# Optimization experiments

Measured on AMD Instinct MI355X. Metric: run time of the kernel, lower is better.

The kernel has to match this reference:

```python
import jax, jax.numpy as jnp
import numpy as np

HIDDEN = 512
HEADS = 8
HEAD_DIM = HIDDEN // HEADS
NUM_NODES = 512
NUM_EDGES = 16384
NEG_INF = -1e9


def setup_inputs() -> dict:
    key = jax.random.key(0)
    ks = jax.random.split(key, 8)
    x = jax.random.normal(ks[0], (4, 12, NUM_NODES, HIDDEN), dtype=jnp.float32)
    edge_index = jax.random.randint(ks[1], (2, NUM_EDGES), 0, NUM_NODES, dtype=jnp.int64)
    s = 1.0 / np.sqrt(HIDDEN)
    Wq = jax.random.uniform(ks[2], (HIDDEN, HIDDEN), jnp.float32, -s, s)
    Wk = jax.random.uniform(ks[3], (HIDDEN, HIDDEN), jnp.float32, -s, s)
    Wv = jax.random.uniform(ks[4], (HIDDEN, HIDDEN), jnp.float32, -s, s)
    bq = jax.random.uniform(ks[5], (HIDDEN,), jnp.float32, -s, s)
    bk = jax.random.uniform(ks[6], (HIDDEN,), jnp.float32, -s, s)
    bv = jax.random.uniform(ks[7], (HIDDEN,), jnp.float32, -s, s)
    return {"x": x, "edge_index": edge_index, "Wq": Wq, "bq": bq,
            "Wk": Wk, "bk": bk, "Wv": Wv, "bv": bv}


def reference(x, edge_index, Wq, bq, Wk, bk, Wv, bv):
    B, S, N, F = x.shape  # [batch, seq_len, num_nodes, features]
    xf = x.reshape(B * S, N, F)
    # torch nn.Linear: y = x @ W.T + b
    Q = xf @ Wq.T + bq
    K = xf @ Wk.T + bk
    V = xf @ Wv.T + bv
    # [B*S, heads, N, head_dim]
    Q = Q.reshape(B * S, N, HEADS, HEAD_DIM).transpose(0, 2, 1, 3)
    K = K.reshape(B * S, N, HEADS, HEAD_DIM).transpose(0, 2, 1, 3)
    V = V.reshape(B * S, N, HEADS, HEAD_DIM).transpose(0, 2, 1, 3)
    scores = jnp.einsum('bhnd,bhmd->bhnm', Q, K) / np.sqrt(HEAD_DIM)
    # static graph mask: 1 where edge exists
    mask = jnp.zeros((N, N), dtype=jnp.float32).at[edge_index[0], edge_index[1]].set(1.0)
    scores = jnp.where(mask[None, None] == 0, NEG_INF, scores)
    attn = jax.nn.softmax(scores, axis=-1)  # dropout is identity in eval
    out = jnp.einsum('bhnm,bhmd->bhnd', attn, V)
    out = out.transpose(0, 2, 1, 3).reshape(B, S, N, F)
    return out
```

## Files before the change

### kernel.cpp

```cpp
#include <hip/hip_runtime.h>
#include <hip/hip_bf16.h>

typedef __attribute__((ext_vector_type(8))) short short8;
typedef __attribute__((ext_vector_type(4))) float f32x4;
typedef __attribute__((ext_vector_type(4))) unsigned int u32x4;
typedef unsigned long long u64;
typedef unsigned short u16;
typedef unsigned int u32;

#define NODES 512
#define HIDDEN 512
#define NEDGES 16384

#define KOFF ((size_t)384 * 32 * 2 * 512)
#define VOFF ((size_t)2 * 384 * 32 * 2 * 512)

static __device__ __forceinline__ u16 f2bf(float f) {
  unsigned u = __float_as_uint(f);
  u += 0x7FFFu + ((u >> 16) & 1u);
  return (u16)(u >> 16);
}

static __device__ __forceinline__ void gld_lds16(const void* g, void* l) {
  __builtin_amdgcn_global_load_lds(
      (const __attribute__((address_space(1))) unsigned int*)g,
      (__attribute__((address_space(3))) unsigned int*)l, 16, 0, 0);
}

__global__ void cast_all(const float* __restrict__ x, const float* __restrict__ wq,
                         const float* __restrict__ wk, const float* __restrict__ wv,
                         u16* __restrict__ xb, u16* __restrict__ wb) {
  const int n4 = 3145728 + 196608;
  int stride = gridDim.x * blockDim.x;
  for (int i = blockIdx.x * blockDim.x + threadIdx.x; i < n4; i += stride) {
    float4 v;
    u16* dst;
    int di;
    if (i < 3145728) {
      v = reinterpret_cast<const float4*>(x)[i];
      dst = xb; di = i;
    } else {
      int t = i - 3145728;
      const float* src = (t < 65536) ? wq : (t < 131072) ? wk : wv;
      v = reinterpret_cast<const float4*>(src)[t & 65535];
      dst = wb; di = t;
    }
    ushort4 o;
    o.x = f2bf(v.x); o.y = f2bf(v.y); o.z = f2bf(v.z); o.w = f2bf(v.w);
    reinterpret_cast<ushort4*>(dst)[di] = o;
  }
}

__global__ void mask_scatter(const int* __restrict__ e, u64* __restrict__ bits) {
  int i = blockIdx.x * blockDim.x + threadIdx.x;
  if (i < NEDGES) {
    int src = e[i];
    int dst = e[NEDGES + i];
    atomicOr(&bits[src * 8 + (dst >> 6)], 1ull << (dst & 63));
  }
}

__global__ void mask_frag(const u64* __restrict__ bits, u32* __restrict__ mf) {
  int idx = blockIdx.x * 256 + threadIdx.x;
  int w = idx & 3;
  int lane = (idx >> 2) & 63;
  int hh = (idx >> 8) & 1;
  int kt = (idx >> 9) & 7;
  int qsg = idx >> 12;
  int q = qsg * 16 + (lane & 15);
  int bit = hh * 32 + (lane >> 4) * 8 + 2 * w;
  u64 row = bits[q * 8 + kt];
  u32 b0 = (u32)(row >> bit) & 1u;
  u32 b1 = (u32)(row >> (bit + 1)) & 1u;
  mf[idx] = (b0 ? 0xFFFFu : 0u) | (b1 ? 0xFFFF0000u : 0u);
}

__global__ __launch_bounds__(256, 2)
void qkv_gemm(const u16* __restrict__ xb, const u16* __restrict__ wb,
              const float* __restrict__ bq, const float* __restrict__ bk,
              const float* __restrict__ bv, u16* __restrict__ qkv) {
  __shared__ u16 As[2][128 * 64];
  __shared__ u16 Bs[2][128 * 64];

  const int blk = blockIdx.x;
  const int xcd = blk & 7;
  const int i = blk >> 3;
  const int m0 = ((i % 24) + xcd * 24) * 128;
  const int nz = i / 24;
  const int n0 = (nz & 3) * 128;
  const int z = nz >> 2;

  const u16* Wz = wb + (size_t)z * (512 * 512);
  const float* bias = (z == 0) ? bq : (z == 1) ? bk : bv;

  const int tid = threadIdx.x;
  const int lane = tid & 63;
  const int w = tid >> 6;
  const int wr = w >> 1, wc = w & 1;
  const int l = lane & 15, j = lane >> 4;
  const int sl = l & 7;
  const int kb = ((lane & 7) ^ (lane >> 3)) * 16;

#define STAGE(bb, kt_) do {                                                     \
    const int k0_ = (kt_) * 64;                                                 \
    _Pragma("unroll")                                                           \
    for (int t_ = 0; t_ < 4; ++t_) {                                            \
      int c_ = w * 4 + t_;                                                      \
      int row_ = c_ * 8 + (lane >> 3);                                          \
      gld_lds16((const char*)xb + ((size_t)(m0 + row_) * 512 + k0_) * 2 + kb,   \
                (char*)&As[bb][0] + c_ * 1024);                                 \
      gld_lds16((const char*)Wz + ((size_t)(n0 + row_) * 512 + k0_) * 2 + kb,   \
                (char*)&Bs[bb][0] + c_ * 1024);                                 \
    }                                                                           \
  } while (0)

  f32x4 acc[4][4] = {};

  STAGE(0, 0);
  int cur = 0;

  for (int kt = 0; kt < 8; ++kt) {
    if (kt < 7) {
      STAGE(cur ^ 1, kt + 1);
      asm volatile("s_waitcnt vmcnt(8)" ::: "memory");
    } else {
      asm volatile("s_waitcnt vmcnt(0)" ::: "memory");
    }
    __builtin_amdgcn_s_barrier();

#pragma unroll
    for (int kk = 0; kk < 2; ++kk) {
      short8 a[4], b[4];
#pragma unroll
      for (int mi = 0; mi < 4; ++mi)
        a[mi] = *(const short8*)(&As[cur][0] + (wr * 64 + mi * 16 + l) * 64 +
                                 (((kk * 4 + j) ^ sl) * 8));
#pragma unroll
      for (int ni = 0; ni < 4; ++ni)
        b[ni] = *(const short8*)(&Bs[cur][0] + (wc * 64 + ni * 16 + l) * 64 +
                                 (((kk * 4 + j) ^ sl) * 8));
      if (z == 2) {
#pragma unroll
        for (int mi = 0; mi < 4; ++mi)
#pragma unroll
          for (int ni = 0; ni < 4; ++ni)
            acc[mi][ni] = __builtin_amdgcn_mfma_f32_16x16x32_bf16(a[mi], b[ni], acc[mi][ni], 0, 0, 0);
      } else {
#pragma unroll
        for (int mi = 0; mi < 4; ++mi)
#pragma unroll
          for (int ni = 0; ni < 4; ++ni)
            acc[mi][ni] = __builtin_amdgcn_mfma_f32_16x16x32_bf16(b[ni], a[mi], acc[mi][ni], 0, 0, 0);
      }
    }

    if (kt < 7) {
      asm volatile("s_waitcnt lgkmcnt(0)" ::: "memory");
      __builtin_amdgcn_s_barrier();
    }
    cur ^= 1;
  }
#undef STAGE

  const int bs = m0 >> 9;
  const int hh = (n0 >> 6) + wc;
  const int bh = bs * 8 + hh;

  if (z == 2) {
    const int ktb = ((m0 & 511) >> 6) + wr;
#pragma unroll
    for (int ni = 0; ni < 4; ++ni) {
      int jcol = n0 + wc * 64 + ni * 16 + l;
      float bv_ = bias[jcol];
      int ds = ni;
#pragma unroll
      for (int mi = 0; mi < 4; ++mi) {
        int kk2 = mi >> 1, oct = ((mi & 1) << 1) | (j >> 1);
        ushort4 pk;
#pragma unroll
        for (int r = 0; r < 4; ++r) pk[r] = f2bf(acc[mi][ni][r] + bv_);
        size_t idx = VOFF + (((((size_t)bh * 8 + ktb) * 2 + kk2) * 4 + ds) * 512)
                   + (oct * 16 + l) * 8 + (j & 1) * 4;
        *reinterpret_cast<ushort4*>(qkv + idx) = pk;
      }
    }
  } else {
#pragma unroll
    for (int ni = 0; ni < 4; ++ni) {
      int n_base = n0 + wc * 64 + ni * 16 + j * 4;
      float4 b4 = *reinterpret_cast<const float4*>(bias + n_base);
      int kk = ni >> 1, oct = ((ni & 1) << 1) | (j >> 1);
#pragma unroll
      for (int mi = 0; mi < 4; ++mi) {
        ushort4 pk;
#pragma unroll
        for (int r = 0; r < 4; ++r) pk[r] = f2bf(acc[mi][ni][r] + (&b4.x)[r]);
        size_t idx;
        if (z == 0) {
          int qsg = ((m0 & 511) >> 4) + wr * 4 + mi;
          idx = ((((size_t)bh * 32 + qsg) * 2 + kk) * 512) + (oct * 16 + l) * 8 + (j & 1) * 4;
        } else {
          int ktb = ((m0 & 511) >> 6) + wr;
          idx = KOFF + (((((size_t)bh * 8 + ktb) * 4 + mi) * 2 + kk) * 512)
              + (oct * 16 + l) * 8 + (j & 1) * 4;
        }
        *reinterpret_cast<ushort4*>(qkv + idx) = pk;
      }
    }
  }
}

__global__ __launch_bounds__(256, 2)
void attn_kernel(const u16* __restrict__ qkv, const u32* __restrict__ mf,
                 float* __restrict__ out) {
  const int blk = blockIdx.x;
  const int xcd = blk & 7;
  const int i = blk >> 3;
  const int bh = xcd * 48 + (i >> 2);
  const int qq = i & 3;
  const int bs = bh >> 3, h = bh & 7;
  const int tid = threadIdx.x;
  const int lane = tid & 63;
  const int w = tid >> 6;
  const int l = lane & 15, j = lane >> 4;
  const int qb = qq * 8 + w * 2;

  short8 qf[2][2];
#pragma unroll
  for (int qs = 0; qs < 2; ++qs)
#pragma unroll
    for (int kk = 0; kk < 2; ++kk)
      qf[qs][kk] = *(const short8*)(qkv + (((size_t)bh * 32 + qb + qs) * 2 + kk) * 512 + lane * 8);

  const u16* Kp = qkv + KOFF + (size_t)bh * 32768 + lane * 8;
  const u16* Vp = qkv + VOFF + (size_t)bh * 32768 + lane * 8;
  const u32* M0 = mf + (qb + 0) * 4096 + lane * 4;
  const u32* M1 = mf + (qb + 1) * 4096 + lane * 4;

  f32x4 o[2][4] = {};
  f32x4 osum[2] = {};
  short8 ones;
#pragma unroll
  for (int t = 0; t < 8; ++t) ones[t] = (short)0x3F80;

#pragma unroll 1
  for (int p = 0; p < 16; ++p) {
    short8 kf2[2][2];
#pragma unroll
    for (int lks = 0; lks < 2; ++lks)
#pragma unroll
      for (int kk = 0; kk < 2; ++kk)
        kf2[lks][kk] = *(const short8*)(Kp + (lks * 2 + kk) * 512);
    short8 vf[4];
#pragma unroll
    for (int ds = 0; ds < 4; ++ds)
      vf[ds] = *(const short8*)(Vp + ds * 512);
    u32x4 am0 = *reinterpret_cast<const u32x4*>(M0);
    u32x4 am1 = *reinterpret_cast<const u32x4*>(M1);

#pragma unroll
    for (int qs = 0; qs < 2; ++qs) {
      f32x4 st[2] = {};
#pragma unroll
      for (int lks = 0; lks < 2; ++lks)
#pragma unroll
        for (int kk = 0; kk < 2; ++kk)
          st[lks] = __builtin_amdgcn_mfma_f32_16x16x32_bf16(
              kf2[lks][kk], qf[qs][kk], st[lks], 0, 0, 0);

      float pr[8];
#pragma unroll
      for (int lks = 0; lks < 2; ++lks)
#pragma unroll
        for (int r = 0; r < 4; ++r)
          pr[lks * 4 + r] = __builtin_exp2f(st[lks][r] * 0.18033688f);
      u32 X0, X1, Y0, Y1;
      asm("v_cvt_pk_bf16_f32 %0, %1, %2" : "=v"(X0) : "v"(pr[0]), "v"(pr[1]));
      asm("v_cvt_pk_bf16_f32 %0, %1, %2" : "=v"(X1) : "v"(pr[2]), "v"(pr[3]));
      asm("v_cvt_pk_bf16_f32 %0, %1, %2" : "=v"(Y0) : "v"(pr[4]), "v"(pr[5]));
      asm("v_cvt_pk_bf16_f32 %0, %1, %2" : "=v"(Y1) : "v"(pr[6]), "v"(pr[7]));
      asm("v_permlane32_swap_b32 %0, %1" : "+v"(X0), "+v"(Y0));
      asm("v_permlane32_swap_b32 %0, %1" : "+v"(X1), "+v"(Y1));
      asm("v_permlane16_swap_b32 %0, %1" : "+v"(X0), "+v"(Y0));
      asm("v_permlane16_swap_b32 %0, %1" : "+v"(X1), "+v"(Y1));
      const u32x4 am = qs ? am1 : am0;
      u32x4 paw;
      paw[0] = X0 & am[0];
      paw[1] = X1 & am[1];
      paw[2] = Y0 & am[2];
      paw[3] = Y1 & am[3];
      short8 pa = __builtin_bit_cast(short8, paw);
      osum[qs] = __builtin_amdgcn_mfma_f32_16x16x32_bf16(pa, ones, osum[qs], 0, 0, 0);
#pragma unroll
      for (int ds = 0; ds < 4; ++ds)
        o[qs][ds] = __builtin_amdgcn_mfma_f32_16x16x32_bf16(pa, vf[ds], o[qs][ds], 0, 0, 0);
    }

    Kp += 2048; Vp += 2048; M0 += 256; M1 += 256;
  }

#pragma unroll
  for (int qs = 0; qs < 2; ++qs) {
    f32x4 inv4;
#pragma unroll
    for (int r = 0; r < 4; ++r) inv4[r] = 1.0f / osum[qs][r];
#pragma unroll
    for (int ds = 0; ds < 4; ++ds) {
      int d = ds * 16 + l;
#pragma unroll
      for (int r = 0; r < 4; ++r) {
        int node = (qb + qs) * 16 + j * 4 + r;
        out[(size_t)bs * 262144 + (size_t)node * 512 + h * 64 + d] = o[qs][ds][r] * inv4[r];
      }
    }
  }
}

extern "C" void kernel_launch(void* const* d_in, const int* in_sizes, int n_in,
                              void* d_out, int out_size, void* d_ws, size_t ws_size,
                              hipStream_t stream) {
  const float* x  = (const float*)d_in[0];
  const int*   e  = (const int*)d_in[1];
  const float* Wq = (const float*)d_in[2];
  const float* bq = (const float*)d_in[3];
  const float* Wk = (const float*)d_in[4];
  const float* bk = (const float*)d_in[5];
  const float* Wv = (const float*)d_in[6];
  const float* bv = (const float*)d_in[7];
  float* out = (float*)d_out;

  char* ws = (char*)d_ws;
  u16* xb   = (u16*)(ws);
  u16* wb   = (u16*)(ws + 25165824);
  u16* qkv  = (u16*)(ws + 26738688);
  u64* mb   = (u64*)(ws + 102236160);
  u32* mfr  = (u32*)(ws + 102268928);

  hipMemsetAsync(mb, 0, 512 * 8 * sizeof(u64), stream);
  mask_scatter<<<(NEDGES + 255) / 256, 256, 0, stream>>>(e, mb);
  mask_frag<<<512, 256, 0, stream>>>(mb, mfr);

  cast_all<<<2048, 256, 0, stream>>>(x, Wq, Wk, Wv, xb, wb);

  qkv_gemm<<<2304, 256, 0, stream>>>(xb, wb, bq, bk, bv, qkv);
  attn_kernel<<<1536, 256, 0, stream>>>(qkv, mfr, out);
}
```

Before: 126.4 us.

## Enlarge QKV GEMM tile to 256x256 with 8 waves and interleaved prefetch

The QKV projection GEMM moves from 128x128 tiles with 4 waves to 256x256 tiles with 8 waves per block. Each wave now holds a 128x64 accumulator, and the next K-slice is loaded in phases interleaved with MFMA sub-steps, with setprio raised around the MFMA bursts. The goal is more data reuse per LDS byte and fewer global loads per FLOP. In exchange it uses 128KB of LDS per block, more registers per thread and fewer blocks (576), which may reduce occupancy and hurt tail balance across CUs.

```diff
diff --git a/kernel.cpp b/kernel.cpp
--- a/kernel.cpp
+++ b/kernel.cpp
@@ -75,107 +75,128 @@
   mf[idx] = (b0 ? 0xFFFFu : 0u) | (b1 ? 0xFFFF0000u : 0u);
 }
 
-__global__ __launch_bounds__(256, 2)
+__global__ __launch_bounds__(512, 2)
 void qkv_gemm(const u16* __restrict__ xb, const u16* __restrict__ wb,
               const float* __restrict__ bq, const float* __restrict__ bk,
               const float* __restrict__ bv, u16* __restrict__ qkv) {
-  __shared__ u16 As[2][128 * 64];
-  __shared__ u16 Bs[2][128 * 64];
+  __shared__ u16 As[2][256 * 64];
+  __shared__ u16 Bs[2][256 * 64];
 
   const int blk = blockIdx.x;
   const int xcd = blk & 7;
   const int i = blk >> 3;
-  const int m0 = ((i % 24) + xcd * 24) * 128;
-  const int nz = i / 24;
-  const int n0 = (nz & 3) * 128;
-  const int z = nz >> 2;
+  const int mt = xcd * 12 + i / 6;
+  const int nz = i % 6;
+  const int m0 = mt * 256;
+  const int n0 = (nz & 1) * 256;
+  const int z  = nz >> 1;
 
   const u16* Wz = wb + (size_t)z * (512 * 512);
   const float* bias = (z == 0) ? bq : (z == 1) ? bk : bv;
 
   const int tid = threadIdx.x;
   const int lane = tid & 63;
-  const int w = tid >> 6;
-  const int wr = w >> 1, wc = w & 1;
+  const int w8 = tid >> 6;
+  const int wr = w8 >> 2, wc = w8 & 3;
   const int l = lane & 15, j = lane >> 4;
   const int sl = l & 7;
-  const int kb = ((lane & 7) ^ (lane >> 3)) * 16;
-
-#define STAGE(bb, kt_) do {                                                     \
-    const int k0_ = (kt_) * 64;                                                 \
-    _Pragma("unroll")                                                           \
-    for (int t_ = 0; t_ < 4; ++t_) {                                            \
-      int c_ = w * 4 + t_;                                                      \
-      int row_ = c_ * 8 + (lane >> 3);                                          \
-      gld_lds16((const char*)xb + ((size_t)(m0 + row_) * 512 + k0_) * 2 + kb,   \
-                (char*)&As[bb][0] + c_ * 1024);                                 \
-      gld_lds16((const char*)Wz + ((size_t)(n0 + row_) * 512 + k0_) * 2 + kb,   \
-                (char*)&Bs[bb][0] + c_ * 1024);                                 \
-    }                                                                           \
-  } while (0)
-
-  f32x4 acc[4][4] = {};
-
-  STAGE(0, 0);
-  int cur = 0;
-
-  for (int kt = 0; kt < 8; ++kt) {
-    if (kt < 7) {
-      STAGE(cur ^ 1, kt + 1);
-      asm volatile("s_waitcnt vmcnt(8)" ::: "memory");
-    } else {
-      asm volatile("s_waitcnt vmcnt(0)" ::: "memory");
-    }
-    __builtin_amdgcn_s_barrier();
-
-#pragma unroll
-    for (int kk = 0; kk < 2; ++kk) {
-      short8 a[4], b[4];
-#pragma unroll
-      for (int mi = 0; mi < 4; ++mi)
-        a[mi] = *(const short8*)(&As[cur][0] + (wr * 64 + mi * 16 + l) * 64 +
-                                 (((kk * 4 + j) ^ sl) * 8));
-#pragma unroll
-      for (int ni = 0; ni < 4; ++ni)
-        b[ni] = *(const short8*)(&Bs[cur][0] + (wc * 64 + ni * 16 + l) * 64 +
-                                 (((kk * 4 + j) ^ sl) * 8));
+  const int swz = ((lane & 7) ^ (lane >> 3)) * 16;
+  const int rsub = lane >> 3;
+
+#define STAGE_A(bb, h, T_) do {                                                  \
+    _Pragma("unroll") for (int q2 = 0; q2 < 2; ++q2) {                           \
+      int row_ = (h) * 128 + q2 * 64 + w8 * 8 + rsub;                            \
+      gld_lds16((const char*)xb + ((size_t)(m0 + row_) * 512 + (T_) * 64) * 2 + swz, \
+                (char*)As + (bb) * 32768 + (h) * 16384 + q2 * 8192 + w8 * 1024); \
+    } } while (0)
+#define STAGE_B(bb, h, T_) do {                                                  \
+    _Pragma("unroll") for (int q2 = 0; q2 < 2; ++q2) {                           \
+      int row_ = (h) * 128 + q2 * 64 + w8 * 8 + rsub;                            \
+      gld_lds16((const char*)Wz + ((size_t)(n0 + row_) * 512 + (T_) * 64) * 2 + swz, \
+                (char*)Bs + (bb) * 32768 + (h) * 16384 + q2 * 8192 + w8 * 1024); \
+    } } while (0)
+
+  f32x4 acc[8][4] = {};
+  short8 Bf[4][2];
+  short8 a[2][2];
+
+  STAGE_A(0, 0, 0); STAGE_A(0, 1, 0); STAGE_B(0, 0, 0); STAGE_B(0, 1, 0);
+  asm volatile("s_waitcnt vmcnt(0)" ::: "memory");
+  __builtin_amdgcn_s_barrier();
+
+#pragma unroll 1
+  for (int T = 0; T < 8; ++T) {
+    const int bc = T & 1;
+    const char* Ab = (const char*)As + bc * 32768;
+    const char* Bb = (const char*)Bs + bc * 32768;
+
+#pragma unroll
+    for (int q = 0; q < 4; ++q) {
+      if (T < 7) {
+        if (q == 0)      { STAGE_A(bc ^ 1, 0, T + 1); STAGE_A(bc ^ 1, 1, T + 1); }
+        else if (q == 1) { STAGE_B(bc ^ 1, 0, T + 1); STAGE_B(bc ^ 1, 1, T + 1); }
+      }
+      if (q == 0) {
+#pragma unroll
+        for (int ni = 0; ni < 4; ++ni)
+#pragma unroll
+          for (int kk = 0; kk < 2; ++kk)
+            Bf[ni][kk] = *(const short8*)(Bb + (wc * 64 + ni * 16 + l) * 128 +
+                                          (((kk * 4 + j) ^ sl) * 16));
+      }
+#pragma unroll
+      for (int mi2 = 0; mi2 < 2; ++mi2)
+#pragma unroll
+        for (int kk = 0; kk < 2; ++kk)
+          a[mi2][kk] = *(const short8*)(Ab + (wr * 128 + (q * 2 + mi2) * 16 + l) * 128 +
+                                        (((kk * 4 + j) ^ sl) * 16));
+
+      __builtin_amdgcn_s_barrier();
+      asm volatile("s_waitcnt lgkmcnt(0)" ::: "memory");
+      __builtin_amdgcn_s_setprio(1);
       if (z == 2) {
 #pragma unroll
-        for (int mi = 0; mi < 4; ++mi)
+        for (int mi2 = 0; mi2 < 2; ++mi2)
 #pragma unroll
           for (int ni = 0; ni < 4; ++ni)
-            acc[mi][ni] = __builtin_amdgcn_mfma_f32_16x16x32_bf16(a[mi], b[ni], acc[mi][ni], 0, 0, 0);
+#pragma unroll
+            for (int kk = 0; kk < 2; ++kk)
+              acc[q * 2 + mi2][ni] = __builtin_amdgcn_mfma_f32_16x16x32_bf16(
+                  a[mi2][kk], Bf[ni][kk], acc[q * 2 + mi2][ni], 0, 0, 0);
       } else {
 #pragma unroll
-        for (int mi = 0; mi < 4; ++mi)
+        for (int mi2 = 0; mi2 < 2; ++mi2)
 #pragma unroll
           for (int ni = 0; ni < 4; ++ni)
-            acc[mi][ni] = __builtin_amdgcn_mfma_f32_16x16x32_bf16(b[ni], a[mi], acc[mi][ni], 0, 0, 0);
-      }
-    }
-
-    if (kt < 7) {
-      asm volatile("s_waitcnt lgkmcnt(0)" ::: "memory");
+#pragma unroll
+            for (int kk = 0; kk < 2; ++kk)
+              acc[q * 2 + mi2][ni] = __builtin_amdgcn_mfma_f32_16x16x32_bf16(
+                  Bf[ni][kk], a[mi2][kk], acc[q * 2 + mi2][ni], 0, 0, 0);
+      }
+      __builtin_amdgcn_s_setprio(0);
+      if (q == 3 && T < 7) {
+        asm volatile("s_waitcnt vmcnt(0)" ::: "memory");
+      }
       __builtin_amdgcn_s_barrier();
     }
-    cur ^= 1;
-  }
-#undef STAGE
+  }
+#undef STAGE_A
+#undef STAGE_B
 
   const int bs = m0 >> 9;
   const int hh = (n0 >> 6) + wc;
   const int bh = bs * 8 + hh;
 
   if (z == 2) {
-    const int ktb = ((m0 & 511) >> 6) + wr;
 #pragma unroll
     for (int ni = 0; ni < 4; ++ni) {
       int jcol = n0 + wc * 64 + ni * 16 + l;
       float bv_ = bias[jcol];
       int ds = ni;
 #pragma unroll
-      for (int mi = 0; mi < 4; ++mi) {
-        int kk2 = mi >> 1, oct = ((mi & 1) << 1) | (j >> 1);
+      for (int mi = 0; mi < 8; ++mi) {
+        int ktb = ((m0 & 511) >> 6) + wr * 2 + (mi >> 2);
+        int kk2 = (mi & 3) >> 1, oct = ((mi & 1) << 1) | (j >> 1);
         ushort4 pk;
 #pragma unroll
         for (int r = 0; r < 4; ++r) pk[r] = f2bf(acc[mi][ni][r] + bv_);
@@ -191,17 +212,18 @@
       float4 b4 = *reinterpret_cast<const float4*>(bias + n_base);
       int kk = ni >> 1, oct = ((ni & 1) << 1) | (j >> 1);
 #pragma unroll
-      for (int mi = 0; mi < 4; ++mi) {
+      for (int mi = 0; mi < 8; ++mi) {
         ushort4 pk;
 #pragma unroll
         for (int r = 0; r < 4; ++r) pk[r] = f2bf(acc[mi][ni][r] + (&b4.x)[r]);
         size_t idx;
         if (z == 0) {
-          int qsg = ((m0 & 511) >> 4) + wr * 4 + mi;
+          int qsg = ((m0 & 511) >> 4) + wr * 8 + mi;
           idx = ((((size_t)bh * 32 + qsg) * 2 + kk) * 512) + (oct * 16 + l) * 8 + (j & 1) * 4;
         } else {
-          int ktb = ((m0 & 511) >> 6) + wr;
-          idx = KOFF + (((((size_t)bh * 8 + ktb) * 4 + mi) * 2 + kk) * 512)
+          int ktb = ((m0 & 511) >> 6) + wr * 2 + (mi >> 2);
+          int ks = mi & 3;
+          idx = KOFF + (((((size_t)bh * 8 + ktb) * 4 + ks) * 2 + kk) * 512)
               + (oct * 16 + l) * 8 + (j & 1) * 4;
         }
         *reinterpret_cast<ushort4*>(qkv + idx) = pk;
@@ -342,6 +364,6 @@
 
   cast_all<<<2048, 256, 0, stream>>>(x, Wq, Wk, Wv, xb, wb);
 
-  qkv_gemm<<<2304, 256, 0, stream>>>(xb, wb, bq, bk, bv, qkv);
+  qkv_gemm<<<576, 512, 0, stream>>>(xb, wb, bq, bk, bv, qkv);
   attn_kernel<<<1536, 256, 0, stream>>>(qkv, mfr, out);
 }
```

Measured after the change: 144.0 us. 13.9% more time.

## Pre-swizzle weights into MFMA fragment layout and load B directly to registers

Applied to the files above, without the earlier changes.

The cast kernel now writes the bf16 weights in a per-lane MFMA fragment order. The QKV GEMM then loads B operands straight from global memory into registers instead of staging them through LDS. This halves LDS traffic and footprint, and removes the B-side shared loads. In exchange, global loads of B are issued per wave with no cross-wave reuse, and the vmcnt accounting is reworked.

```diff
diff --git a/kernel.cpp b/kernel.cpp
--- a/kernel.cpp
+++ b/kernel.cpp
@@ -33,21 +33,25 @@
   const int n4 = 3145728 + 196608;
   int stride = gridDim.x * blockDim.x;
   for (int i = blockIdx.x * blockDim.x + threadIdx.x; i < n4; i += stride) {
-    float4 v;
-    u16* dst;
-    int di;
     if (i < 3145728) {
-      v = reinterpret_cast<const float4*>(x)[i];
-      dst = xb; di = i;
+      float4 v = reinterpret_cast<const float4*>(x)[i];
+      ushort4 o;
+      o.x = f2bf(v.x); o.y = f2bf(v.y); o.z = f2bf(v.z); o.w = f2bf(v.w);
+      reinterpret_cast<ushort4*>(xb)[i] = o;
     } else {
       int t = i - 3145728;
-      const float* src = (t < 65536) ? wq : (t < 131072) ? wk : wv;
-      v = reinterpret_cast<const float4*>(src)[t & 65535];
-      dst = wb; di = t;
-    }
-    ushort4 o;
-    o.x = f2bf(v.x); o.y = f2bf(v.y); o.z = f2bf(v.z); o.w = f2bf(v.w);
-    reinterpret_cast<ushort4*>(dst)[di] = o;
+      int z = t >> 16;
+      int wl = t & 65535;
+      int jrow = wl >> 7;
+      int k = (wl & 127) * 4;
+      const float* src = (z == 0) ? wq : (z == 1) ? wk : wv;
+      float4 v = reinterpret_cast<const float4*>(src)[wl];
+      ushort4 o;
+      o.x = f2bf(v.x); o.y = f2bf(v.y); o.z = f2bf(v.z); o.w = f2bf(v.w);
+      size_t didx = (((size_t)(z * 32 + (jrow >> 4)) * 16 + (k >> 5)) * 64
+                     + (((k >> 3) & 3) * 16 + (jrow & 15))) * 8 + (k & 7);
+      *reinterpret_cast<ushort4*>(wb + didx) = o;
+    }
   }
 }
 
@@ -76,11 +80,10 @@
 }
 
 __global__ __launch_bounds__(256, 2)
-void qkv_gemm(const u16* __restrict__ xb, const u16* __restrict__ wb,
+void qkv_gemm(const u16* __restrict__ xb, const u16* __restrict__ wfrag,
               const float* __restrict__ bq, const float* __restrict__ bk,
               const float* __restrict__ bv, u16* __restrict__ qkv) {
   __shared__ u16 As[2][128 * 64];
-  __shared__ u16 Bs[2][128 * 64];
 
   const int blk = blockIdx.x;
   const int xcd = blk & 7;
@@ -90,7 +93,6 @@
   const int n0 = (nz & 3) * 128;
   const int z = nz >> 2;
 
-  const u16* Wz = wb + (size_t)z * (512 * 512);
   const float* bias = (z == 0) ? bq : (z == 1) ? bk : bv;
 
   const int tid = threadIdx.x;
@@ -101,7 +103,9 @@
   const int sl = l & 7;
   const int kb = ((lane & 7) ^ (lane >> 3)) * 16;
 
-#define STAGE(bb, kt_) do {                                                     \
+  const u16* wf = wfrag + (((size_t)z * 32 + (n0 >> 4) + wc * 4) * 16) * 512 + lane * 8;
+
+#define STAGE_A(bb, kt_) do {                                                   \
     const int k0_ = (kt_) * 64;                                                 \
     _Pragma("unroll")                                                           \
     for (int t_ = 0; t_ < 4; ++t_) {                                            \
@@ -109,48 +113,49 @@
       int row_ = c_ * 8 + (lane >> 3);                                          \
       gld_lds16((const char*)xb + ((size_t)(m0 + row_) * 512 + k0_) * 2 + kb,   \
                 (char*)&As[bb][0] + c_ * 1024);                                 \
-      gld_lds16((const char*)Wz + ((size_t)(n0 + row_) * 512 + k0_) * 2 + kb,   \
-                (char*)&Bs[bb][0] + c_ * 1024);                                 \
     }                                                                           \
   } while (0)
 
   f32x4 acc[4][4] = {};
 
-  STAGE(0, 0);
+  STAGE_A(0, 0);
   int cur = 0;
 
   for (int kt = 0; kt < 8; ++kt) {
+    short8 bf[4][2];
+#pragma unroll
+    for (int ni = 0; ni < 4; ++ni)
+#pragma unroll
+      for (int kk = 0; kk < 2; ++kk)
+        bf[ni][kk] = *(const short8*)(wf + ((ni * 16) + (kt * 2 + kk)) * 512);
+
     if (kt < 7) {
-      STAGE(cur ^ 1, kt + 1);
+      STAGE_A(cur ^ 1, kt + 1);
+      asm volatile("s_waitcnt vmcnt(12)" ::: "memory");
+    } else {
       asm volatile("s_waitcnt vmcnt(8)" ::: "memory");
-    } else {
-      asm volatile("s_waitcnt vmcnt(0)" ::: "memory");
     }
     __builtin_amdgcn_s_barrier();
 
 #pragma unroll
     for (int kk = 0; kk < 2; ++kk) {
-      short8 a[4], b[4];
+      short8 a[4];
 #pragma unroll
       for (int mi = 0; mi < 4; ++mi)
         a[mi] = *(const short8*)(&As[cur][0] + (wr * 64 + mi * 16 + l) * 64 +
                                  (((kk * 4 + j) ^ sl) * 8));
-#pragma unroll
-      for (int ni = 0; ni < 4; ++ni)
-        b[ni] = *(const short8*)(&Bs[cur][0] + (wc * 64 + ni * 16 + l) * 64 +
-                                 (((kk * 4 + j) ^ sl) * 8));
       if (z == 2) {
 #pragma unroll
         for (int mi = 0; mi < 4; ++mi)
 #pragma unroll
           for (int ni = 0; ni < 4; ++ni)
-            acc[mi][ni] = __builtin_amdgcn_mfma_f32_16x16x32_bf16(a[mi], b[ni], acc[mi][ni], 0, 0, 0);
+            acc[mi][ni] = __builtin_amdgcn_mfma_f32_16x16x32_bf16(a[mi], bf[ni][kk], acc[mi][ni], 0, 0, 0);
       } else {
 #pragma unroll
         for (int mi = 0; mi < 4; ++mi)
 #pragma unroll
           for (int ni = 0; ni < 4; ++ni)
-            acc[mi][ni] = __builtin_amdgcn_mfma_f32_16x16x32_bf16(b[ni], a[mi], acc[mi][ni], 0, 0, 0);
+            acc[mi][ni] = __builtin_amdgcn_mfma_f32_16x16x32_bf16(bf[ni][kk], a[mi], acc[mi][ni], 0, 0, 0);
       }
     }
 
@@ -160,7 +165,7 @@
     }
     cur ^= 1;
   }
-#undef STAGE
+#undef STAGE_A
 
   const int bs = m0 >> 9;
   const int hh = (n0 >> 6) + wc;
```

After: 129.1 us. +2.1%, slower.
